# Kernel optimization log

Hardware: AMD Instinct MI355X
Metric: run time of the kernel (lower is better)

The kernel has to match this reference:

```python
import jax, jax.numpy as jnp
import numpy as np
from jax import lax

B, C, D, NH, H, W = 32, 768, 512, 4, 24, 24
HD = C // NH          # 192
FHW = H * W           # 576 (must equal 24*24 per o_proj_img2)


def _p(key, shape, scale=0.02):
    return scale * jax.random.normal(key, shape, dtype=jnp.float32)


def setup_inputs() -> dict:
    ks = jax.random.split(jax.random.key(0), 10)
    return dict(
        img_feats=jax.random.normal(ks[0], (B, C, H, W), jnp.float32),
        txt_feats=jax.random.normal(ks[1], (B, D), jnp.float32),
        fn_w=jnp.ones((C,), jnp.float32), fn_b=jnp.zeros((C,), jnp.float32),
        gn_w=jnp.ones((D,), jnp.float32), gn_b=jnp.zeros((D,), jnp.float32),
        qkv_img_w=_p(ks[2], (3 * C, C)),
        qkv_txt_w=_p(ks[3], (3 * C, D)),
        o_img_w=_p(ks[4], (C, C)), o_img_b=jnp.zeros((C,), jnp.float32),
        o_img2_w=_p(ks[5], (FHW, HD)), o_img2_b=jnp.zeros((FHW,), jnp.float32),
        ffn_norm_w=jnp.ones((C,), jnp.float32), ffn_norm_b=jnp.zeros((C,), jnp.float32),
        fc1_w=_p(ks[6], (C, C)),
        dw_w=_p(ks[7], (C, 1, 3, 3)),
        fc2_w=_p(ks[8], (C, C)),
    )


def layernorm2d(x, w, b, eps=1e-6):
    # normalize over channel dim (dim 1) of NCHW
    u = x.mean(1, keepdims=True)
    s = ((x - u) ** 2).mean(1, keepdims=True)
    x = (x - u) * lax.rsqrt(s + eps)
    return w[:, None, None] * x + b[:, None, None]


def l2norm_last(x, eps=1e-12):
    # F.normalize(x, dim=-1): divide by L2 norm clamped at eps
    n = jnp.sqrt(jnp.sum(x * x, axis=-1, keepdims=True))
    return x / jnp.maximum(n, eps)


def _forward(img_feats, txt_feats, fn_w, fn_b, gn_w, gn_b, qkv_img_w, qkv_txt_w,
             o_img_w, o_img_b, o_img2_w, o_img2_b, ffn_norm_w, ffn_norm_b,
             fc1_w, dw_w, fc2_w):
    x = layernorm2d(img_feats, fn_w, fn_b)
    # guide LayerNorm (torch default eps=1e-5, biased var)
    mu = txt_feats.mean(-1, keepdims=True)
    var = jnp.mean((txt_feats - mu) ** 2, axis=-1, keepdims=True)
    t = (txt_feats - mu) * lax.rsqrt(var + 1e-5) * gn_w + gn_b

    # qkv img: 1x1 conv; channel layout (ng nh hd) -> [B,3,NH,HD,F]
    qkv_img = jnp.einsum('bchw,oc->bohw', x, qkv_img_w).reshape(B, 3, NH, HD, FHW)
    q_img, k_img, v_img = qkv_img[:, 0], qkv_img[:, 1], qkv_img[:, 2]

    # qkv txt: layout 'b (nh (ng hd))' per the two rearranges -> [B,NH,3,HD]
    qkv_txt = (t @ qkv_txt_w.T).reshape(B, NH, 3, HD)
    q_txt, k_txt = qkv_txt[:, :, 0], qkv_txt[:, :, 1]

    # normalize over size-1 trailing dim == x / max(|x|, eps)  (sign-like)
    nq_txt = q_txt / jnp.maximum(jnp.abs(q_txt), 1e-12)          # [B,NH,HD]
    nk_img = l2norm_last(k_img)                                  # [B,NH,HD,F]
    # einsum('bnhd,bnhf->bnhf') with d of size 1 == broadcast multiply over h
    attn1 = jax.nn.softmax(nq_txt[..., None] * nk_img, axis=-1)  # [B,NH,HD,F]
    txt_on_img = jnp.einsum('bnhf,bngf->bnhg', attn1, v_img)     # [B,NH,HD,HD]

    nk_txt = k_txt / jnp.maximum(jnp.abs(k_txt), 1e-12)
    nq_img = l2norm_last(q_img)
    attn2 = jax.nn.softmax(nk_txt[..., None] * nq_img, axis=-1)
    txt_to_img2 = jnp.einsum('bnhf,bngf->bnhg', attn2, v_img)

    img = (txt_on_img + txt_to_img2).reshape(B, NH * HD, HD)     # [B,768,192]
    y = (img @ o_img2_w.T + o_img2_b).reshape(B, C, H, W)        # [B,768,24,24]
    out = jnp.einsum('bchw,oc->bohw', y, o_img_w) + o_img_b[None, :, None, None] + img_feats

    # ConvMlp FFN (mlp_times=1, bias=False convs, exact GELU)
    z = layernorm2d(out, ffn_norm_w, ffn_norm_b)
    z = jnp.einsum('bchw,oc->bohw', z, fc1_w)
    z = lax.conv_general_dilated(z, dw_w, (1, 1), 'SAME',
                                 feature_group_count=C,
                                 dimension_numbers=('NCHW', 'OIHW', 'NCHW'))
    z = jax.nn.gelu(z, approximate=False)
    z = jnp.einsum('bchw,oc->bohw', z, fc2_w)
    return out + z


def reference(img_feats, txt_feats, fn_w, fn_b, gn_w, gn_b, qkv_img_w, qkv_txt_w,
              o_img_w, o_img_b, o_img2_w, o_img2_b, ffn_norm_w, ffn_norm_b,
              fc1_w, dw_w, fc2_w):
    return _forward(img_feats, txt_feats, fn_w, fn_b, gn_w, gn_b, qkv_img_w,
                    qkv_txt_w, o_img_w, o_img_b, o_img2_w, o_img2_b,
                    ffn_norm_w, ffn_norm_b, fc1_w, dw_w, fc2_w)
```

## Files before the change

### kernel.cpp

```cpp
#include <hip/hip_runtime.h>

typedef unsigned short u16;
typedef __attribute__((ext_vector_type(8))) short short8_t;
typedef __attribute__((ext_vector_type(4))) float f32x4;
typedef __attribute__((ext_vector_type(4))) unsigned short u16x4;

static constexpr int cB   = 32;
static constexpr int cC   = 768;
static constexpr int cD   = 512;
static constexpr int cNH  = 4;
static constexpr int cHD  = 192;
static constexpr int cFHW = 576;
static constexpr int cC3  = 2304;

__device__ inline float us2f(u16 s) {
    union { unsigned int u; float f; } v; v.u = ((unsigned int)s) << 16; return v.f;
}
__device__ inline u16 f2bf(float f) {
    union { float f; unsigned int u; } v; v.f = f;
    unsigned int r = v.u + 0x7FFFu + ((v.u >> 16) & 1u);
    return (u16)(r >> 16);
}
__device__ inline float ldflex(const void* p, size_t i, int isf32) {
    return isf32 ? ((const float*)p)[i] : us2f(((const u16*)p)[i]);
}

__device__ inline void gload16(const void* g, void* l) {
    __builtin_amdgcn_global_load_lds(
        (const __attribute__((address_space(1))) void*)g,
        (__attribute__((address_space(3))) void*)l, 16, 0, 0);
}

__global__ void detect_kernel(const u16* __restrict__ raw, int* __restrict__ flags) {
    flags[0] = (raw[0] == 0x3F80u) ? 0 : 1;
}

struct FlatDesc { const void* src[12]; float* dst[12]; int off[13]; };
__global__ __launch_bounds__(256) void flatten_kernel(FlatDesc d, const int* __restrict__ flags) {
    const int isf = flags[0];
    const int gid = blockIdx.x * 256 + threadIdx.x;
    if (gid >= d.off[12]) return;
    int s = 0;
    #pragma unroll
    for (int i = 1; i < 12; i++) s += (gid >= d.off[i]) ? 1 : 0;
    const int j = gid - d.off[s];
    d.dst[s][j] = ldflex(d.src[s], j, isf);
}

__global__ __launch_bounds__(256) void cast_bf16_kernel(
    const void* __restrict__ src, u16* __restrict__ dst, int n, const int* __restrict__ flags)
{
    const int isf = flags[0];
    for (int i = blockIdx.x * 256 + threadIdx.x; i < n; i += gridDim.x * 256)
        dst[i] = isf ? f2bf(((const float*)src)[i]) : ((const u16*)src)[i];
}

__global__ __launch_bounds__(256) void fold_cast_kernel(
    const void* __restrict__ src, const float* __restrict__ gamma,
    u16* __restrict__ dst, int n, const int* __restrict__ flags)
{
    const int isf = flags[0];
    for (int i = blockIdx.x * 256 + threadIdx.x; i < n; i += gridDim.x * 256) {
        const int c = i % cC;
        dst[i] = f2bf(ldflex(src, i, isf) * gamma[c]);
    }
}

__global__ __launch_bounds__(64) void bias_fold_kernel(
    const void* __restrict__ W, const float* __restrict__ gamma, const float* __restrict__ beta,
    float* __restrict__ B1, float* __restrict__ B2, const int* __restrict__ flags)
{
    const int m = blockIdx.x, lane = threadIdx.x, isf = flags[0];
    float s1 = 0.f, s2 = 0.f;
    for (int c = lane; c < cC; c += 64) {
        const float wv = ldflex(W, (size_t)m * cC + c, isf);
        s1 += wv * beta[c]; s2 += wv * gamma[c];
    }
    #pragma unroll
    for (int o = 1; o < 64; o <<= 1) { s1 += __shfl_xor(s1, o, 64); s2 += __shfl_xor(s2, o, 64); }
    if (lane == 0) { B1[m] = s1; B2[m] = s2; }
}

__global__ __launch_bounds__(256) void transpose_kernel(
    const void* __restrict__ src, float* __restrict__ dst,
    int Mdim, int Kdim, const int* __restrict__ flags)
{
    __shared__ float t[32][33];
    const int isf = flags[0];
    const int k0 = blockIdx.x * 32, m0 = blockIdx.y * 32;
    const int x = threadIdx.x & 31, y = threadIdx.x >> 5;
    #pragma unroll
    for (int i = 0; i < 4; i++) {
        const int m = y + i * 8;
        t[m][x] = ldflex(src, (size_t)(m0 + m) * Kdim + k0 + x, isf);
    }
    __syncthreads();
    #pragma unroll
    for (int i = 0; i < 4; i++) {
        const int r = y + i * 8;
        dst[(size_t)(k0 + r) * Mdim + m0 + x] = t[x][r];
    }
}

__global__ __launch_bounds__(256) void txt_ln_kernel(
    const float* __restrict__ txt, const float* __restrict__ gw, const float* __restrict__ gb,
    float* __restrict__ tln)
{
    __shared__ float red[8];
    const int b = blockIdx.x, tid = threadIdx.x;
    const float v0 = txt[(size_t)b * cD + tid];
    const float v1 = txt[(size_t)b * cD + 256 + tid];
    float s = v0 + v1, ss = v0 * v0 + v1 * v1;
    #pragma unroll
    for (int o = 1; o < 64; o <<= 1) { s += __shfl_xor(s, o, 64); ss += __shfl_xor(ss, o, 64); }
    const int wid = tid >> 6, lane = tid & 63;
    if (lane == 0) { red[wid] = s; red[4 + wid] = ss; }
    __syncthreads();
    s  = red[0] + red[1] + red[2] + red[3];
    ss = red[4] + red[5] + red[6] + red[7];
    const float mean = s * (1.f / cD);
    const float var  = fmaxf(ss * (1.f / cD) - mean * mean, 0.f);
    const float r = rsqrtf(var + 1e-5f);
    tln[(size_t)b * cD + tid]       = (v0 - mean) * r * gw[tid]       + gb[tid];
    tln[(size_t)b * cD + 256 + tid] = (v1 - mean) * r * gw[tid + 256] + gb[tid + 256];
}

__global__ __launch_bounds__(256) void txt_gemm_kernel(
    const float* __restrict__ Wt, const float* __restrict__ tln, float* __restrict__ out)
{
    const int o  = blockIdx.x * 256 + threadIdx.x;
    const int b0 = blockIdx.y * 8;
    __shared__ float t[8][cD];
    for (int i = threadIdx.x; i < 8 * cD; i += 256)
        t[i >> 9][i & (cD - 1)] = tln[(size_t)(b0 + (i >> 9)) * cD + (i & (cD - 1))];
    __syncthreads();
    float acc[8] = {};
    #pragma unroll 2
    for (int k = 0; k < cD; k += 4) {
        const float w0 = Wt[(size_t)(k + 0) * cC3 + o];
        const float w1 = Wt[(size_t)(k + 1) * cC3 + o];
        const float w2 = Wt[(size_t)(k + 2) * cC3 + o];
        const float w3 = Wt[(size_t)(k + 3) * cC3 + o];
        #pragma unroll
        for (int b = 0; b < 8; b++) {
            const float4 tv = *(const float4*)&t[b][k];
            acc[b] += w0 * tv.x + w1 * tv.y + w2 * tv.z + w3 * tv.w;
        }
    }
    #pragma unroll
    for (int b = 0; b < 8; b++) out[(size_t)(b0 + b) * cC3 + o] = acc[b];
}

__global__ __launch_bounds__(256) void ln_stats_rows_kernel(
    const u16* __restrict__ Xt, float* __restrict__ mr)
{
    const int wid = threadIdx.x >> 6, lane = threadIdx.x & 63;
    const size_t row = (size_t)blockIdx.x * 4 + wid;
    const u16* r = Xt + row * cC;
    float s = 0.f, ss = 0.f;
    const short8_t a = *(const short8_t*)(r + lane * 8);
    const u16x4 bq   = *(const u16x4*)(r + 512 + lane * 4);
    #pragma unroll
    for (int j = 0; j < 8; j++) { const float v = us2f((u16)a[j]); s += v; ss += v * v; }
    #pragma unroll
    for (int j = 0; j < 4; j++) { const float v = us2f(bq[j]); s += v; ss += v * v; }
    #pragma unroll
    for (int o = 1; o < 64; o <<= 1) { s += __shfl_xor(s, o, 64); ss += __shfl_xor(ss, o, 64); }
    if (lane == 0) {
        const float mean = s * (1.f / cC);
        const float var  = fmaxf(ss * (1.f / cC) - mean * mean, 0.f);
        mr[row * 2] = mean; mr[row * 2 + 1] = rsqrtf(var + 1e-6f);
    }
}

template <int XSRC>
__global__ __launch_bounds__(256) void prep_xt_kernel(
    const void* __restrict__ X, size_t xoff, u16* __restrict__ Xt,
    const int* __restrict__ flags)
{
    __shared__ float t[64][33];
    const int isf = (XSRC == 2) ? flags[0] : 1;
    const int f0 = blockIdx.x * 32, c0 = blockIdx.y * 64, b = blockIdx.z;
    const int tid = threadIdx.x;
    const int fx = tid & 31, cy = tid >> 5;
    const size_t base = (size_t)b * cC * cFHW;
    #pragma unroll
    for (int i = 0; i < 8; i++) {
        const int c = c0 + cy + i * 8;
        const size_t ei = base + (size_t)c * cFHW + f0 + fx;
        t[cy + i * 8][fx] = (XSRC == 2) ? ldflex(X, xoff + ei, isf) : ((const float*)X)[ei];
    }
    __syncthreads();
    const int cx = tid & 31, fy = tid >> 5;
    #pragma unroll
    for (int i = 0; i < 4; i++) {
        const int fl = fy + i * 8;
        const int f = f0 + fl;
        const float v0 = t[cx * 2][fl], v1 = t[cx * 2 + 1][fl];
        const unsigned int pk = (unsigned int)f2bf(v0) | ((unsigned int)f2bf(v1) << 16);
        *(unsigned int*)(Xt + base + (size_t)f * cC + c0 + cx * 2) = pk;
    }
}

template <int EPI>
__global__ __launch_bounds__(256, 2) void conv_mfma(
    const u16* __restrict__ Wb, const u16* __restrict__ Xt,
    float* __restrict__ outp, const float* __restrict__ bias_m,
    const void* __restrict__ resRaw, size_t resOff, const float* __restrict__ resF,
    u16* __restrict__ vout,
    const float* __restrict__ aff_mr, const float* __restrict__ aff_B1, const float* __restrict__ aff_B2,
    int M, int K, int Mt, const int* __restrict__ flags)
{
    const int nwg = 9 * Mt;
    int wg = blockIdx.x;
    {
        const int q = nwg >> 3, r = nwg & 7, x = wg & 7, idx = wg >> 3;
        wg = (x < r ? x * (q + 1) : r * (q + 1) + (x - r) * q) + idx;
    }
    const int xt = wg / Mt, yt = wg - xt * Mt;
    const int n0 = xt * 64, m0 = yt * 256, b = blockIdx.z;

    __shared__ __align__(16) u16 A_s[2][256 * 64];
    __shared__ __align__(16) u16 B_s[2][64 * 64];

    const int tid = threadIdx.x;
    const int w = tid >> 6, lane = tid & 63, lq = lane >> 4, lr = lane & 15;
    const int l8 = lane >> 3, c8 = lane & 7;
    const int xch = ((c8 ^ l8) << 4);

    const u16* wbase = Wb + (size_t)m0 * K;
    const u16* xbase = Xt + ((size_t)b * cFHW + n0) * K;

    f32x4 acc[4][4];
    #pragma unroll
    for (int i = 0; i < 4; i++)
        #pragma unroll
        for (int j = 0; j < 4; j++)
            acc[i][j] = (f32x4)0.f;

    const int nt = K >> 6;

    #pragma unroll
    for (int j = 0; j < 8; ++j) {
        const int r = w * 64 + j * 8 + l8;
        gload16((const char*)(wbase + (size_t)r * K) + xch, (char*)&A_s[0][(w * 64 + j * 8) * 64]);
    }
    #pragma unroll
    for (int j = 0; j < 2; ++j) {
        const int r = w * 16 + j * 8 + l8;
        gload16((const char*)(xbase + (size_t)r * K) + xch, (char*)&B_s[0][(w * 16 + j * 8) * 64]);
    }

    int buf = 0;
    #pragma unroll 1
    for (int t = 0; t < nt; ++t) {
        if (t + 1 < nt) {
            const int k0 = (t + 1) << 6;
            #pragma unroll
            for (int j = 0; j < 8; ++j) {
                const int r = w * 64 + j * 8 + l8;
                gload16((const char*)(wbase + (size_t)r * K + k0) + xch,
                        (char*)&A_s[buf ^ 1][(w * 64 + j * 8) * 64]);
            }
            #pragma unroll
            for (int j = 0; j < 2; ++j) {
                const int r = w * 16 + j * 8 + l8;
                gload16((const char*)(xbase + (size_t)r * K + k0) + xch,
                        (char*)&B_s[buf ^ 1][(w * 16 + j * 8) * 64]);
            }
            asm volatile("s_waitcnt vmcnt(10)" ::: "memory");
        } else {
            asm volatile("s_waitcnt vmcnt(0)" ::: "memory");
        }
        __builtin_amdgcn_s_barrier();
        __builtin_amdgcn_sched_barrier(0);
        __builtin_amdgcn_s_setprio(1);
        const u16* As = &A_s[buf][0];
        const u16* Bs = &B_s[buf][0];
        #pragma unroll
        for (int kk = 0; kk < 2; kk++) {
            short8_t af[4], bfr[4];
            #pragma unroll
            for (int fm = 0; fm < 4; fm++) {
                const int ml = w * 64 + fm * 16 + lr;
                af[fm] = *(const short8_t*)((const char*)As + ml * 128 + ((kk * 64 + lq * 16) ^ ((lr & 7) << 4)));
            }
            #pragma unroll
            for (int fn = 0; fn < 4; fn++) {
                const int nl = fn * 16 + lr;
                bfr[fn] = *(const short8_t*)((const char*)Bs + nl * 128 + ((kk * 64 + lq * 16) ^ ((lr & 7) << 4)));
            }
            #pragma unroll
            for (int fm = 0; fm < 4; fm++)
                #pragma unroll
                for (int fn = 0; fn < 4; fn++)
                    acc[fm][fn] = __builtin_amdgcn_mfma_f32_16x16x32_bf16(af[fm], bfr[fn], acc[fm][fn], 0, 0, 0);
        }
        __builtin_amdgcn_s_setprio(0);
        __builtin_amdgcn_s_barrier();
        buf ^= 1;
    }

    const int mrow0 = m0 + w * 64;

    if constexpr (EPI == 3 || EPI == 4) {
        float b1r[4][4], b2r[4][4];
        #pragma unroll
        for (int fm = 0; fm < 4; fm++)
            #pragma unroll
            for (int i = 0; i < 4; i++) {
                const int mg = mrow0 + fm * 16 + lq * 4 + i;
                b1r[fm][i] = aff_B1[mg];
                b2r[fm][i] = aff_B2[mg];
            }
        #pragma unroll
        for (int fn = 0; fn < 4; fn++) {
            const int nn = n0 + fn * 16 + lr;
            const float2 ms = *(const float2*)(aff_mr + ((size_t)b * cFHW + nn) * 2);
            const float sf = ms.y, mean_sf = ms.x * ms.y;
            #pragma unroll
            for (int fm = 0; fm < 4; fm++)
                #pragma unroll
                for (int i = 0; i < 4; i++) {
                    const int mg = mrow0 + fm * 16 + lq * 4 + i;
                    const float vv = sf * acc[fm][fn][i] + b1r[fm][i] - mean_sf * b2r[fm][i];
                    if constexpr (EPI == 3) {
                        if (m0 >= 2 * cC)
                            vout[((size_t)b * cC + (mg - 2 * cC)) * cFHW + nn] = f2bf(vv);
                        else
                            outp[((size_t)b * 2 * cC + mg) * cFHW + nn] = vv;
                    } else {
                        outp[((size_t)b * M + mg) * cFHW + nn] = vv;
                    }
                }
        }
        return;
    }
    if constexpr (EPI == 1) {
        const int isf = flags[0];
        #pragma unroll
        for (int fm = 0; fm < 4; fm++) {
            #pragma unroll
            for (int fn = 0; fn < 4; fn++) {
                const int nn = n0 + fn * 16 + lr;
                u16x4 pk;
                #pragma unroll
                for (int i = 0; i < 4; i++) {
                    const int mg = mrow0 + fm * 16 + lq * 4 + i;
                    const size_t o = ((size_t)b * M + mg) * cFHW + nn;
                    const float vv = acc[fm][fn][i] + bias_m[mg] + ldflex(resRaw, resOff + o, isf);
                    outp[o] = vv;
                    pk[i] = f2bf(vv);
                }
                *(u16x4*)(vout + ((size_t)b * cFHW + nn) * cC + (mrow0 + fm * 16 + lq * 4)) = pk;
            }
        }
        return;
    }
    #pragma unroll
    for (int fm = 0; fm < 4; fm++) {
        #pragma unroll
        for (int fn = 0; fn < 4; fn++) {
            #pragma unroll
            for (int i = 0; i < 4; i++) {
                const int mg = mrow0 + fm * 16 + lq * 4 + i;
                const size_t o = ((size_t)b * M + mg) * cFHW + n0 + fn * 16 + lr;
                float vv = acc[fm][fn][i];
                if constexpr (EPI == 2) vv += resF[o];
                outp[o] = vv;
            }
        }
    }
}

__global__ __launch_bounds__(64) void attn_p_kernel(
    const float* __restrict__ qk, const float* __restrict__ tq, u16* __restrict__ Pbf)
{
    const int idx = blockIdx.x;
    const int h = idx % cHD;
    const int bn = idx / cHD;
    const int n = bn & 3, b = bn >> 2;
    const int lane = threadIdx.x;
    const float* qrow = qk + ((size_t)b * 2 * cC + n * cHD + h) * cFHW;
    const float* krow = qk + ((size_t)b * 2 * cC + cC + n * cHD + h) * cFHW;
    float kvr[9], qvr[9];
    #pragma unroll
    for (int j = 0; j < 9; j++) {
        kvr[j] = krow[lane + j * 64];
        qvr[j] = qrow[lane + j * 64];
    }
    float ssk = 0.f, mink = 3.0e38f, maxk = -3.0e38f;
    float ssq = 0.f, minq = 3.0e38f, maxq = -3.0e38f;
    #pragma unroll
    for (int j = 0; j < 9; j++) {
        const float kv = kvr[j]; ssk += kv * kv; maxk = fmaxf(maxk, kv); mink = fminf(mink, kv);
        const float qv = qvr[j]; ssq += qv * qv; maxq = fmaxf(maxq, qv); minq = fminf(minq, qv);
    }
    #pragma unroll
    for (int o = 1; o < 64; o <<= 1) {
        ssk += __shfl_xor(ssk, o, 64); ssq += __shfl_xor(ssq, o, 64);
        maxk = fmaxf(maxk, __shfl_xor(maxk, o, 64)); mink = fminf(mink, __shfl_xor(mink, o, 64));
        maxq = fmaxf(maxq, __shfl_xor(maxq, o, 64)); minq = fminf(minq, __shfl_xor(minq, o, 64));
    }
    const float qt = tq[(size_t)b * cC3 + n * 3 * cHD + h];
    const float kt = tq[(size_t)b * cC3 + n * 3 * cHD + cHD + h];
    const float sign1 = qt / fmaxf(fabsf(qt), 1e-12f);
    const float sign2 = kt / fmaxf(fabsf(kt), 1e-12f);
    const float a1 = sign1 / fmaxf(sqrtf(ssk), 1e-12f);
    const float a2 = sign2 / fmaxf(sqrtf(ssq), 1e-12f);
    const float m1 = fmaxf(a1 * maxk, a1 * mink);
    const float m2 = fmaxf(a2 * maxq, a2 * minq);
    float e1[9], e2[9];
    float z1 = 0.f, z2 = 0.f;
    #pragma unroll
    for (int j = 0; j < 9; j++) {
        e1[j] = expf(a1 * kvr[j] - m1); z1 += e1[j];
        e2[j] = expf(a2 * qvr[j] - m2); z2 += e2[j];
    }
    #pragma unroll
    for (int o = 1; o < 64; o <<= 1) { z1 += __shfl_xor(z1, o, 64); z2 += __shfl_xor(z2, o, 64); }
    const float iz1 = 1.f / z1, iz2 = 1.f / z2;
    u16* prow = Pbf + ((size_t)b * cC + n * cHD + h) * cFHW;
    #pragma unroll
    for (int j = 0; j < 9; j++)
        prow[lane + j * 64] = f2bf(e1[j] * iz1 + e2[j] * iz2);
}

__global__ __launch_bounds__(256, 2) void pv_mfma(
    const u16* __restrict__ P, const u16* __restrict__ V, u16* __restrict__ img, int nbn)
{
    const int nwg = 3 * nbn;
    int wg = blockIdx.x;
    {
        const int q = nwg >> 3, r = nwg & 7, x = wg & 7, idx = wg >> 3;
        wg = (x < r ? x * (q + 1) : r * (q + 1) + (x - r) * q) + idx;
    }
    const int bn = wg / 3, gt = wg - bn * 3;
    const int g0 = gt * 64;
    const int b = bn >> 2, n = bn & 3;

    __shared__ __align__(16) u16 A_s[2][192 * 64];
    __shared__ __align__(16) u16 B_s[2][64 * 64];

    const int tid = threadIdx.x;
    const int w = tid >> 6, lane = tid & 63, lq = lane >> 4, lr = lane & 15;
    const int l8 = lane >> 3, c8 = lane & 7;
    const int xch = ((c8 ^ l8) << 4);

    const u16* pbase = P + ((size_t)b * cC + n * cHD) * cFHW;
    const u16* vbase = V + ((size_t)b * cC + n * cHD + g0) * cFHW;

    f32x4 acc[3][4];
    #pragma unroll
    for (int i = 0; i < 3; i++)
        #pragma unroll
        for (int j = 0; j < 4; j++)
            acc[i][j] = (f32x4)0.f;

    const int nt = cFHW / 64;

    #pragma unroll
    for (int j = 0; j < 6; ++j) {
        const int r = w * 48 + j * 8 + l8;
        gload16((const char*)(pbase + (size_t)r * cFHW) + xch, (char*)&A_s[0][(w * 48 + j * 8) * 64]);
    }
    #pragma unroll
    for (int j = 0; j < 2; ++j) {
        const int r = w * 16 + j * 8 + l8;
        gload16((const char*)(vbase + (size_t)r * cFHW) + xch, (char*)&B_s[0][(w * 16 + j * 8) * 64]);
    }

    int buf = 0;
    #pragma unroll 1
    for (int t = 0; t < nt; ++t) {
        if (t + 1 < nt) {
            const int k0 = (t + 1) << 6;
            #pragma unroll
            for (int j = 0; j < 6; ++j) {
                const int r = w * 48 + j * 8 + l8;
                gload16((const char*)(pbase + (size_t)r * cFHW + k0) + xch,
                        (char*)&A_s[buf ^ 1][(w * 48 + j * 8) * 64]);
            }
            #pragma unroll
            for (int j = 0; j < 2; ++j) {
                const int r = w * 16 + j * 8 + l8;
                gload16((const char*)(vbase + (size_t)r * cFHW + k0) + xch,
                        (char*)&B_s[buf ^ 1][(w * 16 + j * 8) * 64]);
            }
            asm volatile("s_waitcnt vmcnt(8)" ::: "memory");
        } else {
            asm volatile("s_waitcnt vmcnt(0)" ::: "memory");
        }
        __builtin_amdgcn_s_barrier();
        __builtin_amdgcn_sched_barrier(0);
        __builtin_amdgcn_s_setprio(1);
        const u16* As = &A_s[buf][0];
        const u16* Bs = &B_s[buf][0];
        #pragma unroll
        for (int kk = 0; kk < 2; kk++) {
            short8_t af[3], bfr[4];
            #pragma unroll
            for (int fm = 0; fm < 3; fm++) {
                const int ml = w * 48 + fm * 16 + lr;
                af[fm] = *(const short8_t*)((const char*)As + ml * 128 + ((kk * 64 + lq * 16) ^ ((lr & 7) << 4)));
            }
            #pragma unroll
            for (int fn = 0; fn < 4; fn++) {
                const int nl = fn * 16 + lr;
                bfr[fn] = *(const short8_t*)((const char*)Bs + nl * 128 + ((kk * 64 + lq * 16) ^ ((lr & 7) << 4)));
            }
            #pragma unroll
            for (int fm = 0; fm < 3; fm++)
                #pragma unroll
                for (int fn = 0; fn < 4; fn++)
                    acc[fm][fn] = __builtin_amdgcn_mfma_f32_16x16x32_bf16(af[fm], bfr[fn], acc[fm][fn], 0, 0, 0);
        }
        __builtin_amdgcn_s_setprio(0);
        __builtin_amdgcn_s_barrier();
        buf ^= 1;
    }

    #pragma unroll
    for (int fm = 0; fm < 3; fm++)
        #pragma unroll
        for (int fn = 0; fn < 4; fn++)
            #pragma unroll
            for (int i = 0; i < 4; i++) {
                const int mm = w * 48 + fm * 16 + lq * 4 + i;
                img[((size_t)b * cC + n * cHD + mm) * cHD + g0 + fn * 16 + lr] = f2bf(acc[fm][fn][i]);
            }
}

__global__ __launch_bounds__(256, 2) void y_mfma(
    const u16* __restrict__ img, const u16* __restrict__ o2w,
    const float* __restrict__ bias_n, u16* __restrict__ Xt)
{
    const int nwg = 9 * 3;
    int wg = blockIdx.x;
    {
        const int q = nwg >> 3, r = nwg & 7, x = wg & 7, idx = wg >> 3;
        wg = (x < r ? x * (q + 1) : r * (q + 1) + (x - r) * q) + idx;
    }
    const int xt = wg / 3, yt = wg - xt * 3;
    const int n0 = xt * 64, m0 = yt * 256, b = blockIdx.z;
    constexpr int K = cHD;

    __shared__ __align__(16) u16 A_s[2][256 * 64];
    __shared__ __align__(16) u16 B_s[2][64 * 64];

    const int tid = threadIdx.x;
    const int w = tid >> 6, lane = tid & 63, lq = lane >> 4, lr = lane & 15;
    const int l8 = lane >> 3, c8 = lane & 7;
    const int xch = ((c8 ^ l8) << 4);

    const u16* abase = img + ((size_t)b * cC + m0) * K;
    const u16* bbase = o2w + (size_t)n0 * K;

    f32x4 acc[4][4];
    #pragma unroll
    for (int i = 0; i < 4; i++)
        #pragma unroll
        for (int j = 0; j < 4; j++)
            acc[i][j] = (f32x4)0.f;

    const int nt = K >> 6;

    #pragma unroll
    for (int j = 0; j < 8; ++j) {
        const int r = w * 64 + j * 8 + l8;
        gload16((const char*)(abase + (size_t)r * K) + xch, (char*)&A_s[0][(w * 64 + j * 8) * 64]);
    }
    #pragma unroll
    for (int j = 0; j < 2; ++j) {
        const int r = w * 16 + j * 8 + l8;
        gload16((const char*)(bbase + (size_t)r * K) + xch, (char*)&B_s[0][(w * 16 + j * 8) * 64]);
    }

    int buf = 0;
    #pragma unroll 1
    for (int t = 0; t < nt; ++t) {
        if (t + 1 < nt) {
            const int k0 = (t + 1) << 6;
            #pragma unroll
            for (int j = 0; j < 8; ++j) {
                const int r = w * 64 + j * 8 + l8;
                gload16((const char*)(abase + (size_t)r * K + k0) + xch,
                        (char*)&A_s[buf ^ 1][(w * 64 + j * 8) * 64]);
            }
            #pragma unroll
            for (int j = 0; j < 2; ++j) {
                const int r = w * 16 + j * 8 + l8;
                gload16((const char*)(bbase + (size_t)r * K + k0) + xch,
                        (char*)&B_s[buf ^ 1][(w * 16 + j * 8) * 64]);
            }
            asm volatile("s_waitcnt vmcnt(10)" ::: "memory");
        } else {
            asm volatile("s_waitcnt vmcnt(0)" ::: "memory");
        }
        __builtin_amdgcn_s_barrier();
        __builtin_amdgcn_sched_barrier(0);
        __builtin_amdgcn_s_setprio(1);
        const u16* As = &A_s[buf][0];
        const u16* Bs = &B_s[buf][0];
        #pragma unroll
        for (int kk = 0; kk < 2; kk++) {
            short8_t af[4], bfr[4];
            #pragma unroll
            for (int fm = 0; fm < 4; fm++) {
                const int ml = w * 64 + fm * 16 + lr;
                af[fm] = *(const short8_t*)((const char*)As + ml * 128 + ((kk * 64 + lq * 16) ^ ((lr & 7) << 4)));
            }
            #pragma unroll
            for (int fn = 0; fn < 4; fn++) {
                const int nl = fn * 16 + lr;
                bfr[fn] = *(const short8_t*)((const char*)Bs + nl * 128 + ((kk * 64 + lq * 16) ^ ((lr & 7) << 4)));
            }
            #pragma unroll
            for (int fm = 0; fm < 4; fm++)
                #pragma unroll
                for (int fn = 0; fn < 4; fn++)
                    acc[fm][fn] = __builtin_amdgcn_mfma_f32_16x16x32_bf16(af[fm], bfr[fn], acc[fm][fn], 0, 0, 0);
        }
        __builtin_amdgcn_s_setprio(0);
        __builtin_amdgcn_s_barrier();
        buf ^= 1;
    }

    #pragma unroll
    for (int fm = 0; fm < 4; fm++) {
        #pragma unroll
        for (int fn = 0; fn < 4; fn++) {
            const int nn = n0 + fn * 16 + lr;
            const float bn_ = bias_n[nn];
            u16x4 pk;
            #pragma unroll
            for (int i = 0; i < 4; i++) pk[i] = f2bf(acc[fm][fn][i] + bn_);
            const int mm = m0 + w * 64 + fm * 16 + lq * 4;
            *(u16x4*)(Xt + ((size_t)b * cFHW + nn) * cC + mm) = pk;
        }
    }
}

__global__ __launch_bounds__(576) void dwconv_gelu_kernel(
    const float* __restrict__ X, const float* __restrict__ w, float* __restrict__ Y)
{
    const int c = blockIdx.x, b = blockIdx.y;
    __shared__ float t[26][28];
    const int tid = threadIdx.x;
    float* tf = &t[0][0];
    for (int i = tid; i < 26 * 28; i += 576) tf[i] = 0.f;
    __syncthreads();
    const size_t base = ((size_t)b * cC + c) * cFHW;
    const int x = tid % 24, y = tid / 24;
    t[y + 1][x + 1] = X[base + tid];
    __syncthreads();
    float w9[9];
    #pragma unroll
    for (int j = 0; j < 9; j++) w9[j] = w[c * 9 + j];
    float s = 0.f;
    #pragma unroll
    for (int dy = 0; dy < 3; dy++)
        #pragma unroll
        for (int dx = 0; dx < 3; dx++)
            s += w9[dy * 3 + dx] * t[y + dy][x + dx];
    const float g = 0.5f * s * (1.f + erff(s * 0.70710678118654752f));
    Y[base + tid] = g;
}

extern "C" void kernel_launch(void* const* d_in, const int* in_sizes, int n_in,
                              void* d_out, int out_size, void* d_ws, size_t ws_size,
                              hipStream_t stream)
{
    char* p = (char*)d_ws;
    auto allocB = [&](size_t bytes) { char* r = p; p += (bytes + 255) & ~(size_t)255; return r; };
    float* c_txt   = (float*)allocB((size_t)cB * cD * 4);
    float* c_fnw   = (float*)allocB(cC * 4);
    float* c_fnb   = (float*)allocB(cC * 4);
    float* c_gnw   = (float*)allocB(cD * 4);
    float* c_gnb   = (float*)allocB(cD * 4);
    float* c_oib   = (float*)allocB(cC * 4);
    float* c_oi2w  = (float*)allocB((size_t)cFHW * cHD * 4);
    float* c_oi2b  = (float*)allocB(cFHW * 4);
    float* c_ffnw  = (float*)allocB(cC * 4);
    float* c_ffnb  = (float*)allocB(cC * 4);
    float* c_dw    = (float*)allocB(cC * 9 * 4);
    u16*   w_qkv_bf = (u16*)allocB((size_t)cC3 * cC * 2);
    u16*   w_oi_bf  = (u16*)allocB((size_t)cC * cC * 2);
    u16*   w_fc1_bf = (u16*)allocB((size_t)cC * cC * 2);
    u16*   w_fc2_bf = (u16*)allocB((size_t)cC * cC * 2);
    u16*   w_o2w_bf = (u16*)allocB((size_t)cFHW * cHD * 2);
    float* t_qkvtw = (float*)allocB((size_t)cD * cC3 * 4);
    float* tln     = (float*)allocB((size_t)cB * cD * 4);
    int*   flags   = (int*)allocB(256);
    float* tq      = (float*)allocB((size_t)cB * cC3 * 4);
    float* mr1     = (float*)allocB((size_t)cB * cFHW * 2 * 4);
    float* mr2     = (float*)allocB((size_t)cB * cFHW * 2 * 4);
    float* b1q     = (float*)allocB(cC3 * 4);
    float* b2q     = (float*)allocB(cC3 * 4);
    float* b1f     = (float*)allocB(cC * 4);
    float* b2f     = (float*)allocB(cC * 4);
    const size_t fixedBytes = (size_t)(p - (char*)d_ws);
    auto needBytes = [&](int Q) {
        return fixedBytes
             + (size_t)Q * cC * cFHW * 4ull * 2ull
             + (size_t)Q * cC * cHD * 2ull
             + (size_t)Q * cC * cFHW * 2ull
             + (size_t)Q * cC * cFHW * 4ull
             + 8192;
    };
    int Q = 8;
    if (ws_size >= needBytes(32)) Q = 32;
    else if (ws_size >= needBytes(16)) Q = 16;
    const size_t QCF = (size_t)Q * cC * cFHW;
    float* slotA = (float*)allocB(2 * QCF * 4);
    u16*   imgbf = (u16*)allocB((size_t)Q * cC * cHD * 2);
    u16*   XtA   = (u16*)allocB(QCF * 2);
    char*  pvreg = allocB(QCF * 4);
    u16*   Pbf = (u16*)pvreg;
    u16*   Vbf = (u16*)(pvreg + QCF * 2);
    float* A0 = slotA, *A1 = slotA + QCF;
    float* A2 = (float*)pvreg;
    (void)in_sizes; (void)n_in; (void)out_size;

    detect_kernel<<<1, 1, 0, stream>>>((const u16*)d_in[2], flags);

    FlatDesc fd;
    const void* srcs[11] = { d_in[1], d_in[2], d_in[3], d_in[4], d_in[5],
                             d_in[9], d_in[10], d_in[11], d_in[12], d_in[13], d_in[15] };
    float* dsts[11]      = { c_txt, c_fnw, c_fnb, c_gnw, c_gnb,
                             c_oib, c_oi2w, c_oi2b, c_ffnw, c_ffnb, c_dw };
    const int ns[11]     = { cB * cD, cC, cC, cD, cD,
                             cC, cFHW * cHD, cFHW, cC, cC, cC * 9 };
    int tot = 0;
    for (int i = 0; i < 11; i++) { fd.src[i] = srcs[i]; fd.dst[i] = dsts[i]; fd.off[i] = tot; tot += ns[i]; }
    fd.src[11] = srcs[0]; fd.dst[11] = dsts[0];
    fd.off[11] = tot; fd.off[12] = tot;
    flatten_kernel<<<(tot + 255) / 256, 256, 0, stream>>>(fd, flags);

    fold_cast_kernel<<<512, 256, 0, stream>>>(d_in[6],  c_fnw,  w_qkv_bf, cC3 * cC, flags);
    cast_bf16_kernel<<<256, 256, 0, stream>>>(d_in[8],  w_oi_bf,  cC * cC, flags);
    fold_cast_kernel<<<256, 256, 0, stream>>>(d_in[14], c_ffnw, w_fc1_bf, cC * cC, flags);
    cast_bf16_kernel<<<256, 256, 0, stream>>>(d_in[16], w_fc2_bf, cC * cC, flags);
    cast_bf16_kernel<<<128, 256, 0, stream>>>(d_in[10], w_o2w_bf, cFHW * cHD, flags);

    bias_fold_kernel<<<cC3, 64, 0, stream>>>(d_in[6],  c_fnw,  c_fnb,  b1q, b2q, flags);
    bias_fold_kernel<<<cC,  64, 0, stream>>>(d_in[14], c_ffnw, c_ffnb, b1f, b2f, flags);

    transpose_kernel<<<dim3(cD / 32, cC3 / 32), 256, 0, stream>>>(d_in[7], t_qkvtw, cC3, cD, flags);
    txt_ln_kernel<<<cB, 256, 0, stream>>>(c_txt, c_gnw, c_gnb, tln);
    txt_gemm_kernel<<<dim3(cC3 / 256, cB / 8), 256, 0, stream>>>(t_qkvtw, tln, tq);

    for (int q0 = 0; q0 < cB; q0 += Q) {
        const size_t off = (size_t)q0 * cC * cFHW;
        u16* XtB = (u16*)((float*)d_out + off);
        prep_xt_kernel<2><<<dim3(cFHW / 32, cC / 64, Q), 256, 0, stream>>>(d_in[0], off, XtA, flags);
        ln_stats_rows_kernel<<<Q * cFHW / 4, 256, 0, stream>>>(XtA, mr1);
        conv_mfma<3><<<dim3(9 * (cC3 / 256), 1, Q), 256, 0, stream>>>(
            w_qkv_bf, XtA, slotA, nullptr, nullptr, 0, nullptr, Vbf,
            mr1, b1q, b2q, cC3, cC, cC3 / 256, flags);
        attn_p_kernel<<<Q * cNH * cHD, 64, 0, stream>>>(slotA, tq + (size_t)q0 * cC3, Pbf);
        pv_mfma<<<3 * Q * cNH, 256, 0, stream>>>(Pbf, Vbf, imgbf, Q * cNH);
        y_mfma<<<dim3(27, 1, Q), 256, 0, stream>>>(imgbf, w_o2w_bf, c_oi2b, XtA);
        conv_mfma<1><<<dim3(9 * (cC / 256), 1, Q), 256, 0, stream>>>(
            w_oi_bf, XtA, A0, c_oib, d_in[0], off, nullptr, XtB,
            nullptr, nullptr, nullptr, cC, cC, cC / 256, flags);
        ln_stats_rows_kernel<<<Q * cFHW / 4, 256, 0, stream>>>(XtB, mr2);
        conv_mfma<4><<<dim3(9 * (cC / 256), 1, Q), 256, 0, stream>>>(
            w_fc1_bf, XtB, A2, nullptr, nullptr, 0, nullptr, nullptr,
            mr2, b1f, b2f, cC, cC, cC / 256, flags);
        dwconv_gelu_kernel<<<dim3(cC, Q), 576, 0, stream>>>(A2, c_dw, A1);
        prep_xt_kernel<0><<<dim3(cFHW / 32, cC / 64, Q), 256, 0, stream>>>(A1, 0, XtA, flags);
        conv_mfma<2><<<dim3(9 * (cC / 256), 1, Q), 256, 0, stream>>>(
            w_fc2_bf, XtA, (float*)d_out + off, nullptr, nullptr, 0, A0, nullptr,
            nullptr, nullptr, nullptr, cC, cC, cC / 256, flags);
    }
}
```

Before: 689.9 us.

## Apply input layernorm before QKV GEMM and store full QKV as bf16

After: 705.0 us. +2.2%, slower.

```diff
diff --git a/kernel.cpp b/kernel.cpp
--- a/kernel.cpp
+++ b/kernel.cpp
@@ -151,6 +151,35 @@
     for (int b = 0; b < 8; b++) out[(size_t)(b0 + b) * cC3 + o] = acc[b];
 }
 
+__global__ __launch_bounds__(1024) void ln_stats_kernel(
+    const void* __restrict__ x, size_t xoff, float* __restrict__ mr,
+    const int* __restrict__ flags)
+{
+    const int isf = flags[0];
+    const int b = blockIdx.y;
+    const int l = threadIdx.x & 63;
+    const int f = (blockIdx.x << 6) + l;
+    const int cg = threadIdx.x >> 6;
+    const size_t base = xoff + (size_t)b * cC * cFHW + f;
+    float s = 0.f, ss = 0.f;
+    for (int c = cg; c < cC; c += 16) {
+        float v = ldflex(x, base + (size_t)c * cFHW, isf);
+        s += v; ss += v * v;
+    }
+    __shared__ float S[16][64], SS[16][64];
+    S[cg][l] = s; SS[cg][l] = ss;
+    __syncthreads();
+    if (threadIdx.x < 64) {
+        float su = 0.f, sq = 0.f;
+        #pragma unroll
+        for (int i = 0; i < 16; i++) { su += S[i][l]; sq += SS[i][l]; }
+        const float mean = su * (1.f / cC);
+        const float var  = fmaxf(sq * (1.f / cC) - mean * mean, 0.f);
+        float* o = mr + ((size_t)b * cFHW + f) * 2;
+        o[0] = mean; o[1] = rsqrtf(var + 1e-6f);
+    }
+}
+
 __global__ __launch_bounds__(256) void ln_stats_rows_kernel(
     const u16* __restrict__ Xt, float* __restrict__ mr)
 {
@@ -176,6 +205,7 @@
 template <int XSRC>
 __global__ __launch_bounds__(256) void prep_xt_kernel(
     const void* __restrict__ X, size_t xoff, u16* __restrict__ Xt,
+    const float* __restrict__ mr, const float* __restrict__ lnw, const float* __restrict__ lnb,
     const int* __restrict__ flags)
 {
     __shared__ float t[64][33];
@@ -196,7 +226,13 @@
     for (int i = 0; i < 4; i++) {
         const int fl = fy + i * 8;
         const int f = f0 + fl;
-        const float v0 = t[cx * 2][fl], v1 = t[cx * 2 + 1][fl];
+        float v0 = t[cx * 2][fl], v1 = t[cx * 2 + 1][fl];
+        if (XSRC == 2) {
+            const float* mp = mr + ((size_t)b * cFHW + f) * 2;
+            const float mean = mp[0], rst = mp[1];
+            v0 = (v0 - mean) * rst * lnw[c0 + cx * 2]     + lnb[c0 + cx * 2];
+            v1 = (v1 - mean) * rst * lnw[c0 + cx * 2 + 1] + lnb[c0 + cx * 2 + 1];
+        }
         const unsigned int pk = (unsigned int)f2bf(v0) | ((unsigned int)f2bf(v1) << 16);
         *(unsigned int*)(Xt + base + (size_t)f * cC + c0 + cx * 2) = pk;
     }
@@ -303,7 +339,19 @@
 
     const int mrow0 = m0 + w * 64;
 
-    if constexpr (EPI == 3 || EPI == 4) {
+    if constexpr (EPI == 5) {
+        #pragma unroll
+        for (int fm = 0; fm < 4; fm++)
+            #pragma unroll
+            for (int fn = 0; fn < 4; fn++)
+                #pragma unroll
+                for (int i = 0; i < 4; i++) {
+                    const int mg = mrow0 + fm * 16 + lq * 4 + i;
+                    vout[((size_t)b * M + mg) * cFHW + n0 + fn * 16 + lr] = f2bf(acc[fm][fn][i]);
+                }
+        return;
+    }
+    if constexpr (EPI == 4) {
         float b1r[4][4], b2r[4][4];
         #pragma unroll
         for (int fm = 0; fm < 4; fm++)
@@ -323,15 +371,8 @@
                 #pragma unroll
                 for (int i = 0; i < 4; i++) {
                     const int mg = mrow0 + fm * 16 + lq * 4 + i;
-                    const float vv = sf * acc[fm][fn][i] + b1r[fm][i] - mean_sf * b2r[fm][i];
-                    if constexpr (EPI == 3) {
-                        if (m0 >= 2 * cC)
-                            vout[((size_t)b * cC + (mg - 2 * cC)) * cFHW + nn] = f2bf(vv);
-                        else
-                            outp[((size_t)b * 2 * cC + mg) * cFHW + nn] = vv;
-                    } else {
-                        outp[((size_t)b * M + mg) * cFHW + nn] = vv;
-                    }
+                    outp[((size_t)b * M + mg) * cFHW + nn] =
+                        sf * acc[fm][fn][i] + b1r[fm][i] - mean_sf * b2r[fm][i];
                 }
         }
         return;
@@ -374,20 +415,20 @@
 }
 
 __global__ __launch_bounds__(64) void attn_p_kernel(
-    const float* __restrict__ qk, const float* __restrict__ tq, u16* __restrict__ Pbf)
+    const u16* __restrict__ qkv, const float* __restrict__ tq, u16* __restrict__ Pbf)
 {
     const int idx = blockIdx.x;
     const int h = idx % cHD;
     const int bn = idx / cHD;
     const int n = bn & 3, b = bn >> 2;
     const int lane = threadIdx.x;
-    const float* qrow = qk + ((size_t)b * 2 * cC + n * cHD + h) * cFHW;
-    const float* krow = qk + ((size_t)b * 2 * cC + cC + n * cHD + h) * cFHW;
+    const u16* qrow = qkv + ((size_t)b * cC3 + n * cHD + h) * cFHW;
+    const u16* krow = qkv + ((size_t)b * cC3 + cC + n * cHD + h) * cFHW;
     float kvr[9], qvr[9];
     #pragma unroll
     for (int j = 0; j < 9; j++) {
-        kvr[j] = krow[lane + j * 64];
-        qvr[j] = qrow[lane + j * 64];
+        kvr[j] = us2f(krow[lane + j * 64]);
+        qvr[j] = us2f(qrow[lane + j * 64]);
     }
     float ssk = 0.f, mink = 3.0e38f, maxk = -3.0e38f;
     float ssq = 0.f, minq = 3.0e38f, maxq = -3.0e38f;
@@ -427,7 +468,7 @@
 }
 
 __global__ __launch_bounds__(256, 2) void pv_mfma(
-    const u16* __restrict__ P, const u16* __restrict__ V, u16* __restrict__ img, int nbn)
+    const u16* __restrict__ P, const u16* __restrict__ qkv, u16* __restrict__ img, int nbn)
 {
     const int nwg = 3 * nbn;
     int wg = blockIdx.x;
@@ -448,7 +489,7 @@
     const int xch = ((c8 ^ l8) << 4);
 
     const u16* pbase = P + ((size_t)b * cC + n * cHD) * cFHW;
-    const u16* vbase = V + ((size_t)b * cC + n * cHD + g0) * cFHW;
+    const u16* vbase = qkv + ((size_t)b * cC3 + 2 * cC + n * cHD + g0) * cFHW;
 
     f32x4 acc[3][4];
     #pragma unroll
@@ -695,31 +736,29 @@
     float* tq      = (float*)allocB((size_t)cB * cC3 * 4);
     float* mr1     = (float*)allocB((size_t)cB * cFHW * 2 * 4);
     float* mr2     = (float*)allocB((size_t)cB * cFHW * 2 * 4);
-    float* b1q     = (float*)allocB(cC3 * 4);
-    float* b2q     = (float*)allocB(cC3 * 4);
     float* b1f     = (float*)allocB(cC * 4);
     float* b2f     = (float*)allocB(cC * 4);
     const size_t fixedBytes = (size_t)(p - (char*)d_ws);
     auto needBytes = [&](int Q) {
         return fixedBytes
+             + (size_t)Q * (cC3 + cC) * cFHW * 2ull
              + (size_t)Q * cC * cFHW * 4ull * 2ull
              + (size_t)Q * cC * cHD * 2ull
              + (size_t)Q * cC * cFHW * 2ull
-             + (size_t)Q * cC * cFHW * 4ull
              + 8192;
     };
     int Q = 8;
     if (ws_size >= needBytes(32)) Q = 32;
     else if (ws_size >= needBytes(16)) Q = 16;
     const size_t QCF = (size_t)Q * cC * cFHW;
-    float* slotA = (float*)allocB(2 * QCF * 4);
+    char*  qkvreg = allocB((size_t)Q * (cC3 + cC) * cFHW * 2);
+    u16*   qkvbf = (u16*)qkvreg;
+    u16*   Pbf   = (u16*)(qkvreg + (size_t)Q * cC3 * cFHW * 2);
+    float* A2    = (float*)qkvreg;
+    float* A0    = (float*)allocB(QCF * 4);
+    float* A1    = (float*)allocB(QCF * 4);
     u16*   imgbf = (u16*)allocB((size_t)Q * cC * cHD * 2);
     u16*   XtA   = (u16*)allocB(QCF * 2);
-    char*  pvreg = allocB(QCF * 4);
-    u16*   Pbf = (u16*)pvreg;
-    u16*   Vbf = (u16*)(pvreg + QCF * 2);
-    float* A0 = slotA, *A1 = slotA + QCF;
-    float* A2 = (float*)pvreg;
     (void)in_sizes; (void)n_in; (void)out_size;
 
     detect_kernel<<<1, 1, 0, stream>>>((const u16*)d_in[2], flags);
@@ -737,14 +776,12 @@
     fd.off[11] = tot; fd.off[12] = tot;
     flatten_kernel<<<(tot + 255) / 256, 256, 0, stream>>>(fd, flags);
 
-    fold_cast_kernel<<<512, 256, 0, stream>>>(d_in[6],  c_fnw,  w_qkv_bf, cC3 * cC, flags);
+    cast_bf16_kernel<<<512, 256, 0, stream>>>(d_in[6],  w_qkv_bf, cC3 * cC, flags);
     cast_bf16_kernel<<<256, 256, 0, stream>>>(d_in[8],  w_oi_bf,  cC * cC, flags);
     fold_cast_kernel<<<256, 256, 0, stream>>>(d_in[14], c_ffnw, w_fc1_bf, cC * cC, flags);
     cast_bf16_kernel<<<256, 256, 0, stream>>>(d_in[16], w_fc2_bf, cC * cC, flags);
     cast_bf16_kernel<<<128, 256, 0, stream>>>(d_in[10], w_o2w_bf, cFHW * cHD, flags);
-
-    bias_fold_kernel<<<cC3, 64, 0, stream>>>(d_in[6],  c_fnw,  c_fnb,  b1q, b2q, flags);
-    bias_fold_kernel<<<cC,  64, 0, stream>>>(d_in[14], c_ffnw, c_ffnb, b1f, b2f, flags);
+    bias_fold_kernel<<<cC, 64, 0, stream>>>(d_in[14], c_ffnw, c_ffnb, b1f, b2f, flags);
 
     transpose_kernel<<<dim3(cD / 32, cC3 / 32), 256, 0, stream>>>(d_in[7], t_qkvtw, cC3, cD, flags);
     txt_ln_kernel<<<cB, 256, 0, stream>>>(c_txt, c_gnw, c_gnb, tln);
@@ -753,13 +790,14 @@
     for (int q0 = 0; q0 < cB; q0 += Q) {
         const size_t off = (size_t)q0 * cC * cFHW;
         u16* XtB = (u16*)((float*)d_out + off);
-        prep_xt_kernel<2><<<dim3(cFHW / 32, cC / 64, Q), 256, 0, stream>>>(d_in[0], off, XtA, flags);
-        ln_stats_rows_kernel<<<Q * cFHW / 4, 256, 0, stream>>>(XtA, mr1);
-        conv_mfma<3><<<dim3(9 * (cC3 / 256), 1, Q), 256, 0, stream>>>(
-            w_qkv_bf, XtA, slotA, nullptr, nullptr, 0, nullptr, Vbf,
-            mr1, b1q, b2q, cC3, cC, cC3 / 256, flags);
-        attn_p_kernel<<<Q * cNH * cHD, 64, 0, stream>>>(slotA, tq + (size_t)q0 * cC3, Pbf);
-        pv_mfma<<<3 * Q * cNH, 256, 0, stream>>>(Pbf, Vbf, imgbf, Q * cNH);
+        ln_stats_kernel<<<dim3(9, Q), 1024, 0, stream>>>(d_in[0], off, mr1, flags);
+        prep_xt_kernel<2><<<dim3(cFHW / 32, cC / 64, Q), 256, 0, stream>>>(
+            d_in[0], off, XtA, mr1, c_fnw, c_fnb, flags);
+        conv_mfma<5><<<dim3(9 * (cC3 / 256), 1, Q), 256, 0, stream>>>(
+            w_qkv_bf, XtA, nullptr, nullptr, nullptr, 0, nullptr, qkvbf,
+            nullptr, nullptr, nullptr, cC3, cC, cC3 / 256, flags);
+        attn_p_kernel<<<Q * cNH * cHD, 64, 0, stream>>>(qkvbf, tq + (size_t)q0 * cC3, Pbf);
+        pv_mfma<<<3 * Q * cNH, 256, 0, stream>>>(Pbf, qkvbf, imgbf, Q * cNH);
         y_mfma<<<dim3(27, 1, Q), 256, 0, stream>>>(imgbf, w_o2w_bf, c_oi2b, XtA);
         conv_mfma<1><<<dim3(9 * (cC / 256), 1, Q), 256, 0, stream>>>(
             w_oi_bf, XtA, A0, c_oib, d_in[0], off, nullptr, XtB,
@@ -769,7 +807,8 @@
             w_fc1_bf, XtB, A2, nullptr, nullptr, 0, nullptr, nullptr,
             mr2, b1f, b2f, cC, cC, cC / 256, flags);
         dwconv_gelu_kernel<<<dim3(cC, Q), 576, 0, stream>>>(A2, c_dw, A1);
-        prep_xt_kernel<0><<<dim3(cFHW / 32, cC / 64, Q), 256, 0, stream>>>(A1, 0, XtA, flags);
+        prep_xt_kernel<0><<<dim3(cFHW / 32, cC / 64, Q), 256, 0, stream>>>(
+            A1, 0, XtA, nullptr, nullptr, nullptr, flags);
         conv_mfma<2><<<dim3(9 * (cC / 256), 1, Q), 256, 0, stream>>>(
             w_fc2_bf, XtA, (float*)d_out + off, nullptr, nullptr, 0, A0, nullptr,
             nullptr, nullptr, nullptr, cC, cC, cC / 256, flags);
```
